# Optimization experiments

Measured on AMD Instinct MI355X. Metric: run time of the kernel, lower is better.

## Reference

```python
import jax, jax.numpy as jnp
import numpy as np

STEP_NUM = 2
SAMPLE_NUM = 10
SAMPLE_SCOPE = 128
NODE_NUM = 232965
INPUT_DIM = 602
HIDDEN_DIM = 256
OUTPUT_DIM = 41
BATCH = 256


def _forward(ids, feature, edge, weight, sample_W, sample_W2, sample_a, W1, W2):
    # a: softmax over the 3 mixing coefficients (matches softmax_a(sample_a) then mm)
    a = jax.nn.softmax(sample_a, axis=0)[:, 0]  # [3]
    key = jax.random.key(42)
    adj_list = [None] * STEP_NUM
    in_nodes = ids
    for i in range(STEP_NUM):
        layer = STEP_NUM - 1 - i
        nbr = edge[in_nodes]              # [n, S] candidate neighbor ids
        src_f = feature[in_nodes]         # [n, F]
        tgt_f = feature[nbr]              # [n, S, F]
        # GAT-style bilinear attention scores (two heads) + structural weight
        s1 = src_f @ sample_W             # [n, H]
        s2 = src_f @ sample_W2            # [n, H]
        t1 = jnp.einsum('nsf,fh->nsh', tgt_f, sample_W)   # [n, S, H]
        t2 = jnp.einsum('nsf,fh->nsh', tgt_f, sample_W2)  # [n, S, H]
        att1 = jnp.einsum('nh,nsh->ns', s1, t1)
        att2 = jnp.einsum('nh,nsh->ns', s2, t2)
        att3 = weight[in_nodes]           # [n, S]
        att = jax.nn.relu(a[0] * att1 + a[1] * att2 + a[2] * att3) + 1e-9
        # Categorical sampling of SAMPLE_NUM neighbors per node
        key, sk = jax.random.split(key)
        cols = jax.random.categorical(sk, jnp.log(att), shape=(SAMPLE_NUM, in_nodes.shape[0])).T  # [n, K]
        # sub-graph adjacency: row-normalized sampled weights (block-sparse structure)
        w = jnp.take_along_axis(weight[in_nodes], cols, axis=1)  # [n, K]
        adj_list[layer] = w / (w.sum(axis=1, keepdims=True) + 1e-9)
        in_nodes = jnp.take_along_axis(nbr, cols, axis=1).reshape(-1)  # [n*K]
    X = feature[in_nodes]                 # start_feat: deepest frontier features
    Ws = [W1, W2]
    for layer in range(STEP_NUM):
        n = adj_list[layer].shape[0]
        # sparse adjacency matmul == per-row weighted sum over sampled neighbors
        X = jnp.einsum('nk,nkd->nd', adj_list[layer], X.reshape(n, SAMPLE_NUM, -1))
        X = X @ Ws[layer]
        if layer < STEP_NUM - 1:
            X = jax.nn.relu(X)  # dropout is identity in eval
    return X


def setup_inputs() -> dict:
    key = jax.random.key(0)
    ks = jax.random.split(key, 9)
    N1 = NODE_NUM + 1
    return {
        'ids': jax.random.randint(ks[0], (BATCH,), 0, NODE_NUM),
        'feature': jax.random.normal(ks[1], (N1, INPUT_DIM), dtype=jnp.float32),
        'edge': jax.random.randint(ks[2], (N1, SAMPLE_SCOPE), 0, NODE_NUM),
        'weight': jax.random.uniform(ks[3], (N1, SAMPLE_SCOPE), dtype=jnp.float32),
        'sample_W': jax.random.normal(ks[4], (INPUT_DIM, HIDDEN_DIM), dtype=jnp.float32) * 0.05,
        'sample_W2': jax.random.normal(ks[5], (INPUT_DIM, HIDDEN_DIM), dtype=jnp.float32) * 0.05,
        'sample_a': jax.random.normal(ks[6], (3, 1), dtype=jnp.float32),
        'W1': jax.random.normal(ks[7], (INPUT_DIM, HIDDEN_DIM), dtype=jnp.float32) * 0.05,
        'W2': jax.random.normal(ks[8], (HIDDEN_DIM, OUTPUT_DIM), dtype=jnp.float32) * 0.05,
    }


def reference(ids, feature, edge, weight, sample_W, sample_W2, sample_a, W1, W2):
    return _forward(ids, feature, edge, weight, sample_W, sample_W2, sample_a, W1, W2)
```

## Files before the change

### kernel.cpp

```cpp
#include <hip/hip_runtime.h>
#include <cstdint>
#include <cstddef>

#define JAX_PARTITIONABLE 1

#define S_SCOPE 128
#define K_SAMP  10
#define F_DIM   602
#define H_DIM   256
#define O_DIM   41
#define BATCH_N 256

__host__ __device__ __forceinline__ void tf2x32(uint32_t k0, uint32_t k1,
                                                uint32_t x0, uint32_t x1,
                                                uint32_t* o0, uint32_t* o1) {
  uint32_t ks2 = k0 ^ k1 ^ 0x1BD11BDAu;
  x0 += k0; x1 += k1;
#define TF_R(d) { x0 += x1; x1 = (x1 << (d)) | (x1 >> (32 - (d))); x1 ^= x0; }
#define TF_G0 TF_R(13) TF_R(15) TF_R(26) TF_R(6)
#define TF_G1 TF_R(17) TF_R(29) TF_R(16) TF_R(24)
  TF_G0; x0 += k1;  x1 += ks2 + 1u;
  TF_G1; x0 += ks2; x1 += k0  + 2u;
  TF_G0; x0 += k0;  x1 += k1  + 3u;
  TF_G1; x0 += k1;  x1 += ks2 + 4u;
  TF_G0; x0 += ks2; x1 += k0  + 5u;
#undef TF_R
#undef TF_G0
#undef TF_G1
  *o0 = x0; *o1 = x1;
}

__device__ __forceinline__ float jax_gumbel(uint32_t ka, uint32_t kb, uint32_t j, uint32_t M) {
  uint32_t r0, r1, bits;
#if JAX_PARTITIONABLE
  tf2x32(ka, kb, 0u, j, &r0, &r1);
  bits = r0 ^ r1;
#else
  uint32_t half = M >> 1;
  if (j < half) { tf2x32(ka, kb, j, j + half, &r0, &r1); bits = r0; }
  else          { tf2x32(ka, kb, j - half, j, &r0, &r1); bits = r1; }
#endif
  float f = __uint_as_float((bits >> 9) | 0x3f800000u) - 1.0f;
  if (f == 0.0f) f = 1.17549435e-38f;
  return -logf(-logf(f));
}

template<int FUSE_Y, int BLK>
__device__ __forceinline__ void att_core(const float* __restrict__ feature,
                                         const float* g1l, const float* g2l,
                                         float* logitl, const float* wtl,
                                         const int* nbrl,
                                         int* coll, float* selw, int* selr,
                                         int nIdx, int n,
                                         float aw0, float aw1, float aw2,
                                         uint32_t ska, uint32_t skb,
                                         float* __restrict__ adj_or_y,
                                         int* __restrict__ out_nodes) {
  constexpr int NW = BLK / 64;
  const int tid = threadIdx.x;
  const int lane = tid & 63;
  const int wave = tid >> 6;

  for (int t16 = 0; t16 < S_SCOPE / (2 * NW); ++t16) {
    const int sA = wave + t16 * (2 * NW);
    const int sB = sA + NW;
    const int nbrA = nbrl[sA];
    const int nbrB = nbrl[sB];
    const float wtA = wtl[sA];
    const float wtB = wtl[sB];
    const float2* frA = (const float2*)(feature + (size_t)nbrA * F_DIM);
    const float2* frB = (const float2*)(feature + (size_t)nbrB * F_DIM);
    float2 vA[5], vB[5], gav[5], gbv[5];
#pragma unroll
    for (int t = 0; t < 5; ++t) {
      const int p = lane + t * 64;
      if (p < F_DIM / 2) {
        vA[t] = frA[p]; vB[t] = frB[p];
        gav[t] = ((const float2*)g1l)[p];
        gbv[t] = ((const float2*)g2l)[p];
      } else {
        vA[t] = make_float2(0.f, 0.f); vB[t] = make_float2(0.f, 0.f);
        gav[t] = make_float2(0.f, 0.f); gbv[t] = make_float2(0.f, 0.f);
      }
    }
    float d1A = 0.f, d2A = 0.f, d1B = 0.f, d2B = 0.f;
#pragma unroll
    for (int t = 0; t < 5; ++t) {
      d1A = fmaf(vA[t].x, gav[t].x, fmaf(vA[t].y, gav[t].y, d1A));
      d2A = fmaf(vA[t].x, gbv[t].x, fmaf(vA[t].y, gbv[t].y, d2A));
      d1B = fmaf(vB[t].x, gav[t].x, fmaf(vB[t].y, gav[t].y, d1B));
      d2B = fmaf(vB[t].x, gbv[t].x, fmaf(vB[t].y, gbv[t].y, d2B));
    }
#pragma unroll
    for (int off = 32; off > 0; off >>= 1) {
      d1A += __shfl_xor(d1A, off); d2A += __shfl_xor(d2A, off);
      d1B += __shfl_xor(d1B, off); d2B += __shfl_xor(d2B, off);
    }
    if (lane == 0) {
      const float attA = fmaxf(aw0 * d1A + aw1 * d2A + aw2 * wtA, 0.0f) + 1e-9f;
      const float attB = fmaxf(aw0 * d1B + aw1 * d2B + aw2 * wtB, 0.0f) + 1e-9f;
      logitl[sA] = logf(attA);
      logitl[sB] = logf(attB);
    }
  }
  __syncthreads();

  const uint32_t M = (uint32_t)K_SAMP * (uint32_t)n * (uint32_t)S_SCOPE;
  for (int k = wave; k < K_SAMP; k += NW) {
    const uint32_t jbase = ((uint32_t)k * (uint32_t)n + (uint32_t)nIdx) * (uint32_t)S_SCOPE;
    float v0 = logitl[lane]      + jax_gumbel(ska, skb, jbase + (uint32_t)lane,        M);
    float v1 = logitl[lane + 64] + jax_gumbel(ska, skb, jbase + (uint32_t)(lane + 64), M);
    float best = v0; int bidx = lane;
    if (v1 > best) { best = v1; bidx = lane + 64; }
#pragma unroll
    for (int off = 1; off < 64; off <<= 1) {
      const float ov = __shfl_xor(best, off);
      const int oi = __shfl_xor(bidx, off);
      if (ov > best || (ov == best && oi < bidx)) { best = ov; bidx = oi; }
    }
    if (lane == 0) coll[k] = bidx;
  }
  __syncthreads();

  if constexpr (FUSE_Y) {
    if (tid == 0) {
      float w[K_SAMP]; float sum = 0.f;
#pragma unroll
      for (int k = 0; k < K_SAMP; ++k) { w[k] = wtl[coll[k]]; sum += w[k]; }
      const float den = sum + 1e-9f;
#pragma unroll
      for (int k = 0; k < K_SAMP; ++k) {
        selw[k] = w[k] / den;
        selr[k] = nbrl[coll[k]];
      }
    }
    __syncthreads();
    for (int e = tid; e < F_DIM; e += BLK) {
      float acc = 0.f;
#pragma unroll
      for (int k = 0; k < K_SAMP; ++k)
        acc = fmaf(selw[k], feature[(size_t)selr[k] * F_DIM + e], acc);
      adj_or_y[(size_t)nIdx * F_DIM + e] = acc;
    }
  } else {
    if (tid == 0) {
      float w[K_SAMP]; float sum = 0.f;
#pragma unroll
      for (int k = 0; k < K_SAMP; ++k) { w[k] = wtl[coll[k]]; sum += w[k]; }
      const float den = sum + 1e-9f;
#pragma unroll
      for (int k = 0; k < K_SAMP; ++k) {
        adj_or_y[(size_t)nIdx * K_SAMP + k] = w[k] / den;
        out_nodes[nIdx * K_SAMP + k] = nbrl[coll[k]];
      }
    }
  }
}

__global__ void __launch_bounds__(512) k_sgatt0(const float* __restrict__ feature,
                                                const int* __restrict__ edge,
                                                const float* __restrict__ weight,
                                                const float* __restrict__ Wa,
                                                const float* __restrict__ Wb,
                                                const int* __restrict__ nodes,
                                                int n,
                                                const float* __restrict__ sample_a,
                                                uint32_t ska, uint32_t skb,
                                                float* __restrict__ adj,
                                                int* __restrict__ out_nodes) {
  __shared__ __align__(16) float fl[604];
  __shared__ __align__(16) float sl[2][H_DIM];
  __shared__ __align__(16) float g1l[604];
  __shared__ __align__(16) float g2l[604];
  __shared__ float logitl[S_SCOPE];
  __shared__ float wtl[S_SCOPE];
  __shared__ int nbrl[S_SCOPE];
  __shared__ int coll[K_SAMP];

  const int nIdx = blockIdx.x;
  const int tid = threadIdx.x;
  const int node = nodes[nIdx];

  const float a0v = sample_a[0], a1v = sample_a[1], a2v = sample_a[2];
  const float mx = fmaxf(a0v, fmaxf(a1v, a2v));
  const float e0 = expf(a0v - mx), e1 = expf(a1v - mx), e2 = expf(a2v - mx);
  const float inv = 1.0f / (e0 + e1 + e2);
  const float aw0 = e0 * inv, aw1 = e1 * inv, aw2 = e2 * inv;

  {
    const float* src = feature + (size_t)node * F_DIM;
    for (int e = tid; e < 604; e += 512) fl[e] = (e < F_DIM) ? src[e] : 0.f;
    if (tid < S_SCOPE) {
      nbrl[tid] = edge[(size_t)node * S_SCOPE + tid];
      wtl[tid] = weight[(size_t)node * S_SCOPE + tid];
    }
  }
  __syncthreads();

  {
    const int head = tid >> 8;
    const int h = tid & 255;
    const float* __restrict__ W = head ? Wb : Wa;
    float a = 0.f;
    for (int fc = 0; fc < 150; ++fc) {
      const int f = fc * 4;
      const float w0 = W[(size_t)(f + 0) * H_DIM + h];
      const float w1 = W[(size_t)(f + 1) * H_DIM + h];
      const float w2 = W[(size_t)(f + 2) * H_DIM + h];
      const float w3 = W[(size_t)(f + 3) * H_DIM + h];
      const float4 v = *(const float4*)&fl[f];
      a = fmaf(v.x, w0, a); a = fmaf(v.y, w1, a);
      a = fmaf(v.z, w2, a); a = fmaf(v.w, w3, a);
    }
    for (int f = 600; f < 602; ++f) a = fmaf(fl[f], W[(size_t)f * H_DIM + h], a);
    sl[head][h] = a;
  }
  __syncthreads();

  for (int j = 0; j < 3; ++j) {
    const int idx = tid + j * 512;
    if (idx < 2 * F_DIM) {
      const int head = idx >= F_DIM;
      const int f = head ? idx - F_DIM : idx;
      const float* __restrict__ W = head ? Wb : Wa;
      const float4* wr = (const float4*)(W + (size_t)f * H_DIM);
      float b = 0.f;
      for (int hq = 0; hq < H_DIM / 4; ++hq) {
        const float4 w = wr[hq];
        const float4 v = *(const float4*)&sl[head][hq * 4];
        b = fmaf(v.x, w.x, b); b = fmaf(v.y, w.y, b);
        b = fmaf(v.z, w.z, b); b = fmaf(v.w, w.w, b);
      }
      (head ? g2l : g1l)[f] = b;
    }
  }
  __syncthreads();

  att_core<0, 512>(feature, g1l, g2l, logitl, wtl, nbrl, coll, nullptr, nullptr,
                   nIdx, n, aw0, aw1, aw2, ska, skb, adj, out_nodes);
}

template<int R>
__global__ void __launch_bounds__(256) k_sg(const float* __restrict__ feature,
                                            const float* __restrict__ Wa,
                                            const float* __restrict__ Wb,
                                            const int* __restrict__ nodes,
                                            float* __restrict__ g1,
                                            float* __restrict__ g2) {
  __shared__ __align__(16) float fl[R][604];
  __shared__ __align__(16) float sl[R][H_DIM];
  const float* __restrict__ W = blockIdx.y ? Wb : Wa;
  float* __restrict__ g = blockIdx.y ? g2 : g1;
  const int r0 = blockIdx.x * R;
  const int tid = threadIdx.x;
  for (int r = 0; r < R; ++r) {
    const float* src = feature + (size_t)nodes[r0 + r] * F_DIM;
    for (int e = tid; e < 604; e += 256) fl[r][e] = (e < F_DIM) ? src[e] : 0.f;
  }
  __syncthreads();

  {
    const int h = tid;
    float a[R];
#pragma unroll
    for (int r = 0; r < R; ++r) a[r] = 0.f;
    for (int fc = 0; fc < 150; ++fc) {
      const int f = fc * 4;
      const float w0 = W[(size_t)(f + 0) * H_DIM + h];
      const float w1 = W[(size_t)(f + 1) * H_DIM + h];
      const float w2 = W[(size_t)(f + 2) * H_DIM + h];
      const float w3 = W[(size_t)(f + 3) * H_DIM + h];
#pragma unroll
      for (int r = 0; r < R; ++r) {
        const float4 v = *(const float4*)&fl[r][f];
        a[r] = fmaf(v.x, w0, a[r]); a[r] = fmaf(v.y, w1, a[r]);
        a[r] = fmaf(v.z, w2, a[r]); a[r] = fmaf(v.w, w3, a[r]);
      }
    }
    for (int f = 600; f < 602; ++f) {
      const float w = W[(size_t)f * H_DIM + h];
#pragma unroll
      for (int r = 0; r < R; ++r) a[r] = fmaf(fl[r][f], w, a[r]);
    }
#pragma unroll
    for (int r = 0; r < R; ++r) sl[r][h] = a[r];
  }
  __syncthreads();

  for (int j = 0; j < 3; ++j) {
    const int f = tid + j * 256;
    if (f < F_DIM) {
      const float4* wr = (const float4*)(W + (size_t)f * H_DIM);
      float b[R];
#pragma unroll
      for (int r = 0; r < R; ++r) b[r] = 0.f;
      for (int hq = 0; hq < H_DIM / 4; ++hq) {
        const float4 w = wr[hq];
#pragma unroll
        for (int r = 0; r < R; ++r) {
          const float4 v = *(const float4*)&sl[r][hq * 4];
          b[r] = fmaf(v.x, w.x, b[r]); b[r] = fmaf(v.y, w.y, b[r]);
          b[r] = fmaf(v.z, w.z, b[r]); b[r] = fmaf(v.w, w.w, b[r]);
        }
      }
#pragma unroll
      for (int r = 0; r < R; ++r)
        g[(size_t)(r0 + r) * F_DIM + f] = b[r];
    }
  }
}

__global__ void __launch_bounds__(512) k_att1(const float* __restrict__ feature,
                                              const int* __restrict__ edge,
                                              const float* __restrict__ weight,
                                              const float* __restrict__ g1,
                                              const float* __restrict__ g2,
                                              const int* __restrict__ nodes,
                                              int n,
                                              const float* __restrict__ sample_a,
                                              uint32_t ska, uint32_t skb,
                                              float* __restrict__ y) {
  __shared__ __align__(16) float g1l[604];
  __shared__ __align__(16) float g2l[604];
  __shared__ float logitl[S_SCOPE];
  __shared__ float wtl[S_SCOPE];
  __shared__ int nbrl[S_SCOPE];
  __shared__ int coll[K_SAMP];
  __shared__ float selw[K_SAMP];
  __shared__ int selr[K_SAMP];

  const int nIdx = blockIdx.x;
  const int tid = threadIdx.x;
  const int node = nodes[nIdx];

  const float a0v = sample_a[0], a1v = sample_a[1], a2v = sample_a[2];
  const float mx = fmaxf(a0v, fmaxf(a1v, a2v));
  const float e0 = expf(a0v - mx), e1 = expf(a1v - mx), e2 = expf(a2v - mx);
  const float inv = 1.0f / (e0 + e1 + e2);
  const float aw0 = e0 * inv, aw1 = e1 * inv, aw2 = e2 * inv;

  for (int e = tid; e < F_DIM; e += 512) {
    g1l[e] = g1[(size_t)nIdx * F_DIM + e];
    g2l[e] = g2[(size_t)nIdx * F_DIM + e];
  }
  if (tid < S_SCOPE) {
    nbrl[tid] = edge[(size_t)node * S_SCOPE + tid];
    wtl[tid] = weight[(size_t)node * S_SCOPE + tid];
  }
  __syncthreads();

  att_core<1, 512>(feature, g1l, g2l, logitl, wtl, nbrl, coll, selw, selr,
                   nIdx, n, aw0, aw1, aw2, ska, skb, y, nullptr);
}

#define HROWS 4
__global__ void __launch_bounds__(256) k_h(const float* __restrict__ y,
                                           const float* __restrict__ W1,
                                           float* __restrict__ H) {
  __shared__ __align__(16) float yl[HROWS][604];
  const int r0 = blockIdx.x * HROWS;
  const int tid = threadIdx.x;
  for (int r = 0; r < HROWS; ++r)
    for (int e = tid; e < 604; e += 256)
      yl[r][e] = (e < F_DIM) ? y[(size_t)(r0 + r) * F_DIM + e] : 0.f;
  __syncthreads();
  const int h = tid;
  float acc[HROWS];
#pragma unroll
  for (int r = 0; r < HROWS; ++r) acc[r] = 0.f;
  for (int fc = 0; fc < 150; ++fc) {
    const int f = fc * 4;
    const float w0 = W1[(size_t)(f + 0) * H_DIM + h];
    const float w1 = W1[(size_t)(f + 1) * H_DIM + h];
    const float w2 = W1[(size_t)(f + 2) * H_DIM + h];
    const float w3 = W1[(size_t)(f + 3) * H_DIM + h];
#pragma unroll
    for (int r = 0; r < HROWS; ++r) {
      const float4 v = *(const float4*)&yl[r][f];
      acc[r] = fmaf(v.x, w0, acc[r]); acc[r] = fmaf(v.y, w1, acc[r]);
      acc[r] = fmaf(v.z, w2, acc[r]); acc[r] = fmaf(v.w, w3, acc[r]);
    }
  }
  for (int f = 600; f < 602; ++f) {
    const float w = W1[(size_t)f * H_DIM + h];
#pragma unroll
    for (int r = 0; r < HROWS; ++r) acc[r] = fmaf(yl[r][f], w, acc[r]);
  }
#pragma unroll
  for (int r = 0; r < HROWS; ++r)
    H[(size_t)(r0 + r) * H_DIM + h] = fmaxf(acc[r], 0.f);
}

__global__ void __launch_bounds__(256) k_final(const float* __restrict__ H,
                                               const float* __restrict__ adj1,
                                               const float* __restrict__ W2,
                                               float* __restrict__ out) {
  __shared__ float zl[H_DIM];
  const int nIdx = blockIdx.x;
  const int tid = threadIdx.x;
  float acc = 0.f;
#pragma unroll
  for (int k = 0; k < K_SAMP; ++k)
    acc = fmaf(adj1[(size_t)nIdx * K_SAMP + k],
               H[(size_t)(nIdx * K_SAMP + k) * H_DIM + tid], acc);
  zl[tid] = acc;
  __syncthreads();
  if (tid < O_DIM) {
    float o = 0.f;
    for (int hh = 0; hh < H_DIM; ++hh)
      o = fmaf(zl[hh], W2[(size_t)hh * O_DIM + tid], o);
    out[(size_t)nIdx * O_DIM + tid] = o;
  }
}

extern "C" void kernel_launch(void* const* d_in, const int* in_sizes, int n_in,
                              void* d_out, int out_size, void* d_ws, size_t ws_size,
                              hipStream_t stream) {
  (void)in_sizes; (void)n_in; (void)out_size; (void)ws_size;
  const int*   ids       = (const int*)d_in[0];
  const float* feature   = (const float*)d_in[1];
  const int*   edge      = (const int*)d_in[2];
  const float* weight    = (const float*)d_in[3];
  const float* sample_W  = (const float*)d_in[4];
  const float* sample_W2 = (const float*)d_in[5];
  const float* sample_a  = (const float*)d_in[6];
  const float* W1        = (const float*)d_in[7];
  const float* W2        = (const float*)d_in[8];
  float* out = (float*)d_out;

  const int N1 = BATCH_N;
  const int N2 = BATCH_N * K_SAMP;

  float* ws   = (float*)d_ws;
  float* g1   = ws;
  float* g2   = g1 + (size_t)N2 * F_DIM;
  float* yb   = g2 + (size_t)N2 * F_DIM;
  float* Hb   = yb + (size_t)N2 * F_DIM;
  float* adj1 = Hb + (size_t)N2 * H_DIM;
  int*   in1  = (int*)(adj1 + (size_t)N1 * K_SAMP);

  uint32_t k0 = 0u, k1 = 42u;
  uint32_t nk0, nk1, sk0a, sk0b, sk1a, sk1b;
#if JAX_PARTITIONABLE
  {
    tf2x32(k0, k1, 0u, 0u, &nk0, &nk1);
    tf2x32(k0, k1, 0u, 1u, &sk0a, &sk0b);
    tf2x32(nk0, nk1, 0u, 1u, &sk1a, &sk1b);
  }
#else
  {
    uint32_t a0, b0, a1, b1;
    tf2x32(k0, k1, 0u, 2u, &a0, &b0);
    tf2x32(k0, k1, 1u, 3u, &a1, &b1);
    nk0 = a0; nk1 = a1; sk0a = b0; sk0b = b1;
    tf2x32(nk0, nk1, 0u, 2u, &a0, &b0);
    tf2x32(nk0, nk1, 1u, 3u, &a1, &b1);
    sk1a = b0; sk1b = b1;
  }
#endif

  k_sgatt0<<<N1, 512, 0, stream>>>(feature, edge, weight, sample_W, sample_W2,
                                   ids, N1, sample_a, sk0a, sk0b, adj1, in1);
  k_sg<10><<<dim3(N2 / 10, 2), 256, 0, stream>>>(feature, sample_W, sample_W2, in1, g1, g2);
  k_att1<<<N2, 512, 0, stream>>>(feature, edge, weight, g1, g2, in1, N2,
                                 sample_a, sk1a, sk1b, yb);
  k_h<<<N2 / HROWS, 256, 0, stream>>>(yb, W1, Hb);
  k_final<<<N1, 256, 0, stream>>>(Hb, adj1, W2, out);
}
```

Measured before the change: 380.3 us.

## Split layer-1 attention into parallel scoring kernel and separate sampling kernel

Replaces the fused k_att1 kernel (one block per node, each wave scoring 16 neighbors serially) with k_score, a 2D grid where each wave scores a single neighbor. A separate k_samp kernel then does Gumbel sampling and feature aggregation from logits stored in a new workspace buffer. The aim is more parallelism and more outstanding gather loads for the dominant random-feature-read phase. The cost is an extra launch, a logits round trip through global memory, and g1/g2 being reloaded into shared memory by 16 blocks per node instead of once.

```diff
diff --git a/kernel.cpp b/kernel.cpp
--- a/kernel.cpp
+++ b/kernel.cpp
@@ -45,66 +45,22 @@
   return -logf(-logf(f));
 }
 
-template<int FUSE_Y, int BLK>
-__device__ __forceinline__ void att_core(const float* __restrict__ feature,
-                                         const float* g1l, const float* g2l,
-                                         float* logitl, const float* wtl,
-                                         const int* nbrl,
-                                         int* coll, float* selw, int* selr,
-                                         int nIdx, int n,
-                                         float aw0, float aw1, float aw2,
-                                         uint32_t ska, uint32_t skb,
-                                         float* __restrict__ adj_or_y,
-                                         int* __restrict__ out_nodes) {
-  constexpr int NW = BLK / 64;
+__device__ __forceinline__ void mix_a(const float* __restrict__ sample_a,
+                                      float& aw0, float& aw1, float& aw2) {
+  const float a0v = sample_a[0], a1v = sample_a[1], a2v = sample_a[2];
+  const float mx = fmaxf(a0v, fmaxf(a1v, a2v));
+  const float e0 = expf(a0v - mx), e1 = expf(a1v - mx), e2 = expf(a2v - mx);
+  const float inv = 1.0f / (e0 + e1 + e2);
+  aw0 = e0 * inv; aw1 = e1 * inv; aw2 = e2 * inv;
+}
+
+template<int NW>
+__device__ __forceinline__ void sample_phase(const float* logitl, int* coll,
+                                             int nIdx, int n,
+                                             uint32_t ska, uint32_t skb) {
   const int tid = threadIdx.x;
   const int lane = tid & 63;
   const int wave = tid >> 6;
-
-  for (int t16 = 0; t16 < S_SCOPE / (2 * NW); ++t16) {
-    const int sA = wave + t16 * (2 * NW);
-    const int sB = sA + NW;
-    const int nbrA = nbrl[sA];
-    const int nbrB = nbrl[sB];
-    const float wtA = wtl[sA];
-    const float wtB = wtl[sB];
-    const float2* frA = (const float2*)(feature + (size_t)nbrA * F_DIM);
-    const float2* frB = (const float2*)(feature + (size_t)nbrB * F_DIM);
-    float2 vA[5], vB[5], gav[5], gbv[5];
-#pragma unroll
-    for (int t = 0; t < 5; ++t) {
-      const int p = lane + t * 64;
-      if (p < F_DIM / 2) {
-        vA[t] = frA[p]; vB[t] = frB[p];
-        gav[t] = ((const float2*)g1l)[p];
-        gbv[t] = ((const float2*)g2l)[p];
-      } else {
-        vA[t] = make_float2(0.f, 0.f); vB[t] = make_float2(0.f, 0.f);
-        gav[t] = make_float2(0.f, 0.f); gbv[t] = make_float2(0.f, 0.f);
-      }
-    }
-    float d1A = 0.f, d2A = 0.f, d1B = 0.f, d2B = 0.f;
-#pragma unroll
-    for (int t = 0; t < 5; ++t) {
-      d1A = fmaf(vA[t].x, gav[t].x, fmaf(vA[t].y, gav[t].y, d1A));
-      d2A = fmaf(vA[t].x, gbv[t].x, fmaf(vA[t].y, gbv[t].y, d2A));
-      d1B = fmaf(vB[t].x, gav[t].x, fmaf(vB[t].y, gav[t].y, d1B));
-      d2B = fmaf(vB[t].x, gbv[t].x, fmaf(vB[t].y, gbv[t].y, d2B));
-    }
-#pragma unroll
-    for (int off = 32; off > 0; off >>= 1) {
-      d1A += __shfl_xor(d1A, off); d2A += __shfl_xor(d2A, off);
-      d1B += __shfl_xor(d1B, off); d2B += __shfl_xor(d2B, off);
-    }
-    if (lane == 0) {
-      const float attA = fmaxf(aw0 * d1A + aw1 * d2A + aw2 * wtA, 0.0f) + 1e-9f;
-      const float attB = fmaxf(aw0 * d1B + aw1 * d2B + aw2 * wtB, 0.0f) + 1e-9f;
-      logitl[sA] = logf(attA);
-      logitl[sB] = logf(attB);
-    }
-  }
-  __syncthreads();
-
   const uint32_t M = (uint32_t)K_SAMP * (uint32_t)n * (uint32_t)S_SCOPE;
   for (int k = wave; k < K_SAMP; k += NW) {
     const uint32_t jbase = ((uint32_t)k * (uint32_t)n + (uint32_t)nIdx) * (uint32_t)S_SCOPE;
@@ -120,40 +76,115 @@
     }
     if (lane == 0) coll[k] = bidx;
   }
-  __syncthreads();
-
-  if constexpr (FUSE_Y) {
-    if (tid == 0) {
-      float w[K_SAMP]; float sum = 0.f;
-#pragma unroll
-      for (int k = 0; k < K_SAMP; ++k) { w[k] = wtl[coll[k]]; sum += w[k]; }
-      const float den = sum + 1e-9f;
-#pragma unroll
-      for (int k = 0; k < K_SAMP; ++k) {
-        selw[k] = w[k] / den;
-        selr[k] = nbrl[coll[k]];
-      }
-    }
-    __syncthreads();
-    for (int e = tid; e < F_DIM; e += BLK) {
-      float acc = 0.f;
-#pragma unroll
-      for (int k = 0; k < K_SAMP; ++k)
-        acc = fmaf(selw[k], feature[(size_t)selr[k] * F_DIM + e], acc);
-      adj_or_y[(size_t)nIdx * F_DIM + e] = acc;
-    }
-  } else {
-    if (tid == 0) {
-      float w[K_SAMP]; float sum = 0.f;
-#pragma unroll
-      for (int k = 0; k < K_SAMP; ++k) { w[k] = wtl[coll[k]]; sum += w[k]; }
-      const float den = sum + 1e-9f;
-#pragma unroll
-      for (int k = 0; k < K_SAMP; ++k) {
-        adj_or_y[(size_t)nIdx * K_SAMP + k] = w[k] / den;
-        out_nodes[nIdx * K_SAMP + k] = nbrl[coll[k]];
-      }
-    }
+}
+
+__global__ void __launch_bounds__(512) k_score(const float* __restrict__ feature,
+                                               const int* __restrict__ edge,
+                                               const float* __restrict__ weight,
+                                               const float* __restrict__ g1,
+                                               const float* __restrict__ g2,
+                                               const int* __restrict__ nodes,
+                                               const float* __restrict__ sample_a,
+                                               float* __restrict__ logits) {
+  __shared__ __align__(16) float g1l[604];
+  __shared__ __align__(16) float g2l[604];
+  const int nIdx = blockIdx.x;
+  const int tid = threadIdx.x;
+  const int lane = tid & 63;
+  const int wave = tid >> 6;
+  const int s = blockIdx.y * 8 + wave;
+  const int node = nodes[nIdx];
+
+  float aw0, aw1, aw2;
+  mix_a(sample_a, aw0, aw1, aw2);
+
+  for (int e = tid; e < F_DIM; e += 512) {
+    g1l[e] = g1[(size_t)nIdx * F_DIM + e];
+    g2l[e] = g2[(size_t)nIdx * F_DIM + e];
+  }
+  __syncthreads();
+
+  const int nbr = edge[(size_t)node * S_SCOPE + s];
+  const float wt = weight[(size_t)node * S_SCOPE + s];
+  const float2* fr = (const float2*)(feature + (size_t)nbr * F_DIM);
+  float2 vA[5], gav[5], gbv[5];
+#pragma unroll
+  for (int t = 0; t < 5; ++t) {
+    const int p = lane + t * 64;
+    if (p < F_DIM / 2) {
+      vA[t] = fr[p];
+      gav[t] = ((const float2*)g1l)[p];
+      gbv[t] = ((const float2*)g2l)[p];
+    } else {
+      vA[t] = make_float2(0.f, 0.f);
+      gav[t] = make_float2(0.f, 0.f);
+      gbv[t] = make_float2(0.f, 0.f);
+    }
+  }
+  float d1 = 0.f, d2 = 0.f;
+#pragma unroll
+  for (int t = 0; t < 5; ++t) {
+    d1 = fmaf(vA[t].x, gav[t].x, fmaf(vA[t].y, gav[t].y, d1));
+    d2 = fmaf(vA[t].x, gbv[t].x, fmaf(vA[t].y, gbv[t].y, d2));
+  }
+#pragma unroll
+  for (int off = 32; off > 0; off >>= 1) {
+    d1 += __shfl_xor(d1, off);
+    d2 += __shfl_xor(d2, off);
+  }
+  if (lane == 0) {
+    const float att = fmaxf(aw0 * d1 + aw1 * d2 + aw2 * wt, 0.0f) + 1e-9f;
+    logits[(size_t)nIdx * S_SCOPE + s] = logf(att);
+  }
+}
+
+__global__ void __launch_bounds__(512) k_samp(const float* __restrict__ feature,
+                                              const int* __restrict__ edge,
+                                              const float* __restrict__ weight,
+                                              const float* __restrict__ logits,
+                                              const int* __restrict__ nodes,
+                                              int n,
+                                              uint32_t ska, uint32_t skb,
+                                              float* __restrict__ y) {
+  __shared__ float logitl[S_SCOPE];
+  __shared__ float wtl[S_SCOPE];
+  __shared__ int nbrl[S_SCOPE];
+  __shared__ int coll[K_SAMP];
+  __shared__ float selw[K_SAMP];
+  __shared__ int selr[K_SAMP];
+
+  const int nIdx = blockIdx.x;
+  const int tid = threadIdx.x;
+  const int node = nodes[nIdx];
+
+  if (tid < S_SCOPE) {
+    logitl[tid] = logits[(size_t)nIdx * S_SCOPE + tid];
+    nbrl[tid] = edge[(size_t)node * S_SCOPE + tid];
+    wtl[tid] = weight[(size_t)node * S_SCOPE + tid];
+  }
+  __syncthreads();
+
+  sample_phase<8>(logitl, coll, nIdx, n, ska, skb);
+  __syncthreads();
+
+  if (tid == 0) {
+    float w[K_SAMP]; float sum = 0.f;
+#pragma unroll
+    for (int k = 0; k < K_SAMP; ++k) { w[k] = wtl[coll[k]]; sum += w[k]; }
+    const float den = sum + 1e-9f;
+#pragma unroll
+    for (int k = 0; k < K_SAMP; ++k) {
+      selw[k] = w[k] / den;
+      selr[k] = nbrl[coll[k]];
+    }
+  }
+  __syncthreads();
+  for (int e = tid; e < F_DIM; e += 512) {
+    float acc = 0.f;
+#pragma unroll
+    for (int k = 0; k < K_SAMP; ++k)
+      acc = fmaf(selw[k], feature[(size_t)selr[k] * F_DIM + e], acc);
+    y[(size_t)nIdx * F_DIM + e] = acc;
   }
 }
 
@@ -179,13 +210,12 @@
 
   const int nIdx = blockIdx.x;
   const int tid = threadIdx.x;
+  const int lane = tid & 63;
+  const int wave = tid >> 6;
   const int node = nodes[nIdx];
 
-  const float a0v = sample_a[0], a1v = sample_a[1], a2v = sample_a[2];
-  const float mx = fmaxf(a0v, fmaxf(a1v, a2v));
-  const float e0 = expf(a0v - mx), e1 = expf(a1v - mx), e2 = expf(a2v - mx);
-  const float inv = 1.0f / (e0 + e1 + e2);
-  const float aw0 = e0 * inv, aw1 = e1 * inv, aw2 = e2 * inv;
+  float aw0, aw1, aw2;
+  mix_a(sample_a, aw0, aw1, aw2);
 
   {
     const float* src = feature + (size_t)node * F_DIM;
@@ -236,8 +266,64 @@
   }
   __syncthreads();
 
-  att_core<0, 512>(feature, g1l, g2l, logitl, wtl, nbrl, coll, nullptr, nullptr,
-                   nIdx, n, aw0, aw1, aw2, ska, skb, adj, out_nodes);
+  for (int t16 = 0; t16 < S_SCOPE / 16; ++t16) {
+    const int sA = wave + t16 * 16;
+    const int sB = sA + 8;
+    const int nbrA = nbrl[sA];
+    const int nbrB = nbrl[sB];
+    const float wtA = wtl[sA];
+    const float wtB = wtl[sB];
+    const float2* frA = (const float2*)(feature + (size_t)nbrA * F_DIM);
+    const float2* frB = (const float2*)(feature + (size_t)nbrB * F_DIM);
+    float2 vA[5], vB[5], gav[5], gbv[5];
+#pragma unroll
+    for (int t = 0; t < 5; ++t) {
+      const int p = lane + t * 64;
+      if (p < F_DIM / 2) {
+        vA[t] = frA[p]; vB[t] = frB[p];
+        gav[t] = ((const float2*)g1l)[p];
+        gbv[t] = ((const float2*)g2l)[p];
+      } else {
+        vA[t] = make_float2(0.f, 0.f); vB[t] = make_float2(0.f, 0.f);
+        gav[t] = make_float2(0.f, 0.f); gbv[t] = make_float2(0.f, 0.f);
+      }
+    }
+    float d1A = 0.f, d2A = 0.f, d1B = 0.f, d2B = 0.f;
+#pragma unroll
+    for (int t = 0; t < 5; ++t) {
+      d1A = fmaf(vA[t].x, gav[t].x, fmaf(vA[t].y, gav[t].y, d1A));
+      d2A = fmaf(vA[t].x, gbv[t].x, fmaf(vA[t].y, gbv[t].y, d2A));
+      d1B = fmaf(vB[t].x, gav[t].x, fmaf(vB[t].y, gav[t].y, d1B));
+      d2B = fmaf(vB[t].x, gbv[t].x, fmaf(vB[t].y, gbv[t].y, d2B));
+    }
+#pragma unroll
+    for (int off = 32; off > 0; off >>= 1) {
+      d1A += __shfl_xor(d1A, off); d2A += __shfl_xor(d2A, off);
+      d1B += __shfl_xor(d1B, off); d2B += __shfl_xor(d2B, off);
+    }
+    if (lane == 0) {
+      const float attA = fmaxf(aw0 * d1A + aw1 * d2A + aw2 * wtA, 0.0f) + 1e-9f;
+      const float attB = fmaxf(aw0 * d1B + aw1 * d2B + aw2 * wtB, 0.0f) + 1e-9f;
+      logitl[sA] = logf(attA);
+      logitl[sB] = logf(attB);
+    }
+  }
+  __syncthreads();
+
+  sample_phase<8>(logitl, coll, nIdx, n, ska, skb);
+  __syncthreads();
+
+  if (tid == 0) {
+    float w[K_SAMP]; float sum = 0.f;
+#pragma unroll
+    for (int k = 0; k < K_SAMP; ++k) { w[k] = wtl[coll[k]]; sum += w[k]; }
+    const float den = sum + 1e-9f;
+#pragma unroll
+    for (int k = 0; k < K_SAMP; ++k) {
+      adj[(size_t)nIdx * K_SAMP + k] = w[k] / den;
+      out_nodes[nIdx * K_SAMP + k] = nbrl[coll[k]];
+    }
+  }
 }
 
 template<int R>
@@ -308,49 +394,6 @@
         g[(size_t)(r0 + r) * F_DIM + f] = b[r];
     }
   }
-}
-
-__global__ void __launch_bounds__(512) k_att1(const float* __restrict__ feature,
-                                              const int* __restrict__ edge,
-                                              const float* __restrict__ weight,
-                                              const float* __restrict__ g1,
-                                              const float* __restrict__ g2,
-                                              const int* __restrict__ nodes,
-                                              int n,
-                                              const float* __restrict__ sample_a,
-                                              uint32_t ska, uint32_t skb,
-                                              float* __restrict__ y) {
-  __shared__ __align__(16) float g1l[604];
-  __shared__ __align__(16) float g2l[604];
-  __shared__ float logitl[S_SCOPE];
-  __shared__ float wtl[S_SCOPE];
-  __shared__ int nbrl[S_SCOPE];
-  __shared__ int coll[K_SAMP];
-  __shared__ float selw[K_SAMP];
-  __shared__ int selr[K_SAMP];
-
-  const int nIdx = blockIdx.x;
-  const int tid = threadIdx.x;
-  const int node = nodes[nIdx];
-
-  const float a0v = sample_a[0], a1v = sample_a[1], a2v = sample_a[2];
-  const float mx = fmaxf(a0v, fmaxf(a1v, a2v));
-  const float e0 = expf(a0v - mx), e1 = expf(a1v - mx), e2 = expf(a2v - mx);
-  const float inv = 1.0f / (e0 + e1 + e2);
-  const float aw0 = e0 * inv, aw1 = e1 * inv, aw2 = e2 * inv;
-
-  for (int e = tid; e < F_DIM; e += 512) {
-    g1l[e] = g1[(size_t)nIdx * F_DIM + e];
-    g2l[e] = g2[(size_t)nIdx * F_DIM + e];
-  }
-  if (tid < S_SCOPE) {
-    nbrl[tid] = edge[(size_t)node * S_SCOPE + tid];
-    wtl[tid] = weight[(size_t)node * S_SCOPE + tid];
-  }
-  __syncthreads();
-
-  att_core<1, 512>(feature, g1l, g2l, logitl, wtl, nbrl, coll, selw, selr,
-                   nIdx, n, aw0, aw1, aw2, ska, skb, y, nullptr);
 }
 
 #define HROWS 4
@@ -431,13 +474,14 @@
   const int N1 = BATCH_N;
   const int N2 = BATCH_N * K_SAMP;
 
-  float* ws   = (float*)d_ws;
-  float* g1   = ws;
-  float* g2   = g1 + (size_t)N2 * F_DIM;
-  float* yb   = g2 + (size_t)N2 * F_DIM;
-  float* Hb   = yb + (size_t)N2 * F_DIM;
-  float* adj1 = Hb + (size_t)N2 * H_DIM;
-  int*   in1  = (int*)(adj1 + (size_t)N1 * K_SAMP);
+  float* ws     = (float*)d_ws;
+  float* g1     = ws;
+  float* g2     = g1 + (size_t)N2 * F_DIM;
+  float* yb     = g2 + (size_t)N2 * F_DIM;
+  float* Hb     = yb + (size_t)N2 * F_DIM;
+  float* adj1   = Hb + (size_t)N2 * H_DIM;
+  float* logits = adj1 + (size_t)N1 * K_SAMP;
+  int*   in1    = (int*)(logits + (size_t)N2 * S_SCOPE);
 
   uint32_t k0 = 0u, k1 = 42u;
   uint32_t nk0, nk1, sk0a, sk0b, sk1a, sk1b;
@@ -462,8 +506,10 @@
   k_sgatt0<<<N1, 512, 0, stream>>>(feature, edge, weight, sample_W, sample_W2,
                                    ids, N1, sample_a, sk0a, sk0b, adj1, in1);
   k_sg<10><<<dim3(N2 / 10, 2), 256, 0, stream>>>(feature, sample_W, sample_W2, in1, g1, g2);
-  k_att1<<<N2, 512, 0, stream>>>(feature, edge, weight, g1, g2, in1, N2,
-                                 sample_a, sk1a, sk1b, yb);
+  k_score<<<dim3(N2, S_SCOPE / 8), 512, 0, stream>>>(feature, edge, weight, g1, g2,
+                                                     in1, sample_a, logits);
+  k_samp<<<N2, 512, 0, stream>>>(feature, edge, weight, logits, in1, N2,
+                                 sk1a, sk1b, yb);
   k_h<<<N2 / HROWS, 256, 0, stream>>>(yb, W1, Hb);
   k_final<<<N1, 256, 0, stream>>>(Hb, adj1, W2, out);
 }
```

Result: slower. 429.1 us (+12.8%).
